# Performance work log

Measured on AMD Instinct MI355X. Metric: run time of the kernel, lower is better.

The kernel has to match this reference:

```python
import jax, jax.numpy as jnp
import numpy as np
from jax import lax

B, CIN, HID, T, H, W = 4, 16, 16, 31, 128, 128


def setup_inputs() -> dict:
    key = jax.random.key(0)
    k1, k2 = jax.random.split(key)
    X = jax.random.normal(k1, (B, CIN, T, H, W), dtype=jnp.float32)
    # conv weight: Conv3d(in=16, out=4*hidden=64, k=3, pad=1), fan-in scaled
    fan_in = CIN * 27
    Wt = jax.random.normal(k2, (4 * HID, CIN, 3, 3, 3), dtype=jnp.float32) / np.sqrt(fan_in)
    b = jnp.zeros((4 * HID,), dtype=jnp.float32)
    return {"X": X, "W": Wt, "b": b}


def reference(X, W, b):
    # conv step: [B, 4*HID, T, H, W]
    gates = lax.conv_general_dilated(
        X, W, window_strides=(1, 1, 1), padding="SAME",
        dimension_numbers=("NCDHW", "OIDHW", "NCDHW"))
    gates = gates + b[None, :, None, None, None]
    Z, F, O, I = jnp.split(gates, 4, axis=1)
    Z = jnp.tanh(Z)
    F = jax.nn.sigmoid(F)
    O = jax.nn.sigmoid(O)
    I = jax.nn.sigmoid(I)

    # linear recurrence over time (axis=2), forward direction:
    # c_t = f_t * c_{t-1} + i_t * z_t  (c_{-1} = 0), h_t = o_t * c_t
    Zt = jnp.moveaxis(Z, 2, 0)  # [T, B, HID, H, W]
    Ft = jnp.moveaxis(F, 2, 0)
    Ot = jnp.moveaxis(O, 2, 0)
    It = jnp.moveaxis(I, 2, 0)

    def step(c, zfio):
        z, f, o, i = zfio
        c_ = f * c + i * z
        return c_, o * c_

    c0 = jnp.zeros_like(Zt[0])
    _, hs = lax.scan(step, c0, (Zt, Ft, Ot, It))
    return jnp.moveaxis(hs, 0, 2)  # [B, HID, T, H, W]
```

## Files before the change

kernel.cpp:

```cpp
#include <hip/hip_runtime.h>
#include <math.h>

#define Bn   4
#define CINn 16
#define HIDn 16
#define Tn   31
#define Hn   128
#define Wn   128

#define NS   14

typedef _Float16 half8 __attribute__((ext_vector_type(8)));
typedef float    f32x4 __attribute__((ext_vector_type(4)));

constexpr int KDt[28] = {0,0,0,0,0,0,0,0,0, 1,1,1,1,1,1,1,1,1, 2,2,2,2,2,2,2,2,2, 2};
constexpr int KHt[28] = {0,0,0,1,1,1,2,2,2, 0,0,0,1,1,1,2,2,2, 0,0,0,1,1,1,2,2,2, 2};
constexpr int KWt[28] = {0,1,2,0,1,2,0,1,2, 0,1,2,0,1,2,0,1,2, 0,1,2,0,1,2,0,1,2, 2};

__device__ __forceinline__ float sigmoidf_(float x) { return 1.f / (1.f + __expf(-x)); }
__device__ __forceinline__ float tanhf_(float x)    { return 2.f / (1.f + __expf(-2.f * x)) - 1.f; }

__global__ void repack_wa_kernel(const float* __restrict__ W, _Float16* __restrict__ WA) {
    int idx = blockIdx.x * blockDim.x + threadIdx.x;
    if (idx >= NS * 4 * 64 * 8) return;
    int j    = idx & 7;
    int lane = (idx >> 3) & 63;
    int m    = (idx >> 9) & 3;
    int s    = idx >> 11;
    int g    = lane >> 4;
    int tap  = 2 * s + (g >> 1);
    int cin  = (g & 1) * 8 + j;
    int oc   = m * 16 + (lane & 15);
    float v  = (tap < 27) ? W[(size_t)(oc * CINn + cin) * 27 + tap] : 0.f;
    WA[idx] = (_Float16)v;
}

#define POSB    48
#define NWPOS   66
#define ROWF    (NWPOS*POSB)
#define SLOTF   (3*ROWF)
#define LDSF    (4*SLOTF)
#define NPOS    (3*NWPOS)
#define XH_OFF  65536
#define SLICE_B (Hn*Wn*CINn*2)
#define WS_NEED ((size_t)XH_OFF + (size_t)Bn*Tn*SLICE_B)

__global__ __launch_bounds__(256)
void transpose_x_kernel(const float* __restrict__ X, _Float16* __restrict__ Xh) {
    int i   = blockIdx.x * 256 + threadIdx.x;
    int pos = i & 16383;
    int bu  = i >> 14;
    int b   = bu / 31;
    int u   = bu - b * 31;
    const float* src = X + ((size_t)(b * CINn) * Tn + u) * 16384 + pos;
    half8 h0, h1;
    #pragma unroll
    for (int c = 0; c < 8; c++) h0[c] = (_Float16)src[(size_t)c * (Tn * 16384)];
    #pragma unroll
    for (int c = 0; c < 8; c++) h1[c] = (_Float16)src[(size_t)(c + 8) * (Tn * 16384)];
    half8* dst = (half8*)(Xh + (size_t)i * 16);
    dst[0] = h0; dst[1] = h1;
}

__global__ __launch_bounds__(256, 2)
void qrnn_xh_kernel(const _Float16* __restrict__ Xh, const _Float16* __restrict__ WA,
                    const float* __restrict__ bias, float* __restrict__ out) {
    __shared__ __align__(16) char smem[LDSF];

    const int tid  = threadIdx.x;
    const int lane = tid & 63;
    const int wv   = tid >> 6;

    const int swz = (blockIdx.x & 7) * 128 + (blockIdx.x >> 3);
    const int b    = swz >> 8;
    const int h    = (swz >> 1) & 127;
    const int wh   = swz & 1;
    const int woff = wh * 64;

    const size_t strideT = (size_t)Hn * Wn;
    const size_t strideC = (size_t)Tn * strideT;

    const int lane15 = lane & 15;
    const int g      = lane >> 4;
    const int ghi    = g >> 1;
    const int e      = g & 1;
    const int wloc   = wv * 16 + lane15;
    const int pbase  = wloc * POSB + e * 16;

    float bz[4], bfv[4], bov[4], biv[4];
    #pragma unroll
    for (int r = 0; r < 4; r++) {
        int hid = g * 4 + r;
        bz[r]  = bias[hid];
        bfv[r] = bias[HIDn + hid];
        bov[r] = bias[2 * HIDn + hid];
        biv[r] = bias[3 * HIDn + hid];
    }

    const char* XhB = (const char*)Xh + (size_t)b * Tn * SLICE_B;
    const bool own  = (tid < NPOS);
    const int  srow = tid / NWPOS;
    const int  swp  = tid - srow * NWPOS;
    const int  hr   = h - 1 + srow;
    const int  wa   = woff - 1 + swp;
    const bool inb  = own && (hr >= 0) && (hr < Hn) && (wa >= 0) && (wa < Wn);
    const int  soff = (hr * Wn + wa) * 32;
    const int  loff = srow * ROWF + swp * POSB;

    half8 pfA, pfB;

    auto issue = [&](int u) {
        half8 a = {}, c = {};
        if (inb && u >= 0 && u < Tn) {
            const char* s = XhB + (size_t)u * SLICE_B + soff;
            a = *reinterpret_cast<const half8*>(s);
            c = *reinterpret_cast<const half8*>(s + 16);
        }
        pfA = a; pfB = c;
    };
    auto commit = [&](int u) {
        if (own) {
            char* dst = smem + (u & 3) * SLOTF + loff;
            *reinterpret_cast<half8*>(dst)      = pfA;
            *reinterpret_cast<half8*>(dst + 16) = pfB;
        }
    };

    if (own) {
        half8 z = {};
        char* dst = smem + 3 * SLOTF + loff;
        *reinterpret_cast<half8*>(dst)      = z;
        *reinterpret_cast<half8*>(dst + 16) = z;
    }
    issue(0);
    commit(0);
    issue(1);

    float cst[4] = {0.f, 0.f, 0.f, 0.f};
    float* outb = out + (size_t)b * HIDn * strideC + (size_t)h * Wn + woff + wloc;

    for (int t = 0; t < Tn; t++) {
        commit(t + 1);
        __syncthreads();
        issue(t + 2);

        const int sb[3] = { ((t + 3) & 3) * SLOTF, (t & 3) * SLOTF, ((t + 1) & 3) * SLOTF };

        f32x4 acc[4];
        #pragma unroll
        for (int m = 0; m < 4; m++) acc[m] = (f32x4)(0.f);

        #pragma unroll
        for (int s = 0; s < NS; s++) {
            const half8 a0 = *reinterpret_cast<const half8*>(WA + ((size_t)(s * 4 + 0) * 64 + lane) * 8);
            const half8 a1 = *reinterpret_cast<const half8*>(WA + ((size_t)(s * 4 + 1) * 64 + lane) * 8);
            const half8 a2 = *reinterpret_cast<const half8*>(WA + ((size_t)(s * 4 + 2) * 64 + lane) * 8);
            const half8 a3 = *reinterpret_cast<const half8*>(WA + ((size_t)(s * 4 + 3) * 64 + lane) * 8);

            const int tA = 2 * s, tB = 2 * s + 1;
            const int offA = sb[KDt[tA]] + KHt[tA] * ROWF + KWt[tA] * POSB;
            const int offB = sb[KDt[tB]] + KHt[tB] * ROWF + KWt[tB] * POSB;
            const int off  = (ghi ? offB : offA) + pbase;

            const half8 bf = *reinterpret_cast<const half8*>(smem + off);
            acc[0] = __builtin_amdgcn_mfma_f32_16x16x32_f16(a0, bf, acc[0], 0, 0, 0);
            acc[1] = __builtin_amdgcn_mfma_f32_16x16x32_f16(a1, bf, acc[1], 0, 0, 0);
            acc[2] = __builtin_amdgcn_mfma_f32_16x16x32_f16(a2, bf, acc[2], 0, 0, 0);
            acc[3] = __builtin_amdgcn_mfma_f32_16x16x32_f16(a3, bf, acc[3], 0, 0, 0);
        }

        #pragma unroll
        for (int r = 0; r < 4; r++) {
            float z = tanhf_   (acc[0][r] + bz[r]);
            float f = sigmoidf_(acc[1][r] + bfv[r]);
            float o = sigmoidf_(acc[2][r] + bov[r]);
            float i = sigmoidf_(acc[3][r] + biv[r]);
            float c = f * cst[r] + i * z;
            cst[r] = c;
            outb[(size_t)(g * 4 + r) * strideC + (size_t)t * strideT] = o * c;
        }
    }
}

#define WSTR  48
#define ROWB  (130*WSTR)
#define SLOT3 (3*ROWB)
#define LDS3  (3*SLOT3)

__global__ __launch_bounds__(256, 2)
void qrnn_fb_kernel(const float* __restrict__ X, const _Float16* __restrict__ WA,
                    const float* __restrict__ bias, float* __restrict__ out) {
    __shared__ __align__(16) char smem[LDS3];
    const int tid  = threadIdx.x;
    const int lane = tid & 63;
    const int wv   = tid >> 6;
    const int swz = (blockIdx.x & 7) * 64 + (blockIdx.x >> 3);
    const int b = swz >> 7;
    const int h = swz & 127;
    const size_t strideT = (size_t)Hn * Wn;
    const size_t strideC = (size_t)Tn * strideT;
    const float* Xb = X + (size_t)b * CINn * strideC;
    const int lane15  = lane & 15;
    const int g       = lane >> 4;
    const int ghi     = g >> 1;
    const int laneoff = lane15 * WSTR + (g & 1) * 16;
    const int wbase   = wv * 32;
    float bz[4], bfv[4], bov[4], biv[4];
    #pragma unroll
    for (int r = 0; r < 4; r++) {
        int hid = g * 4 + r;
        bz[r] = bias[hid]; bfv[r] = bias[HIDn + hid];
        bov[r] = bias[2 * HIDn + hid]; biv[r] = bias[3 * HIDn + hid];
    }
    auto stage = [&](int u, int s) {
        const bool uok = (u >= 0) && (u < Tn);
        for (int p = tid; p < 3 * 130; p += 256) {
            int row  = (p >= 260) ? 2 : (p >= 130) ? 1 : 0;
            int wpos = p - row * 130;
            int hr = h - 1 + row;
            int wa = wpos - 1;
            bool valid = uok && (hr >= 0) && (hr < Hn) && (wa >= 0) && (wa < Wn);
            const float* src = Xb + (ptrdiff_t)u * (ptrdiff_t)strideT + (ptrdiff_t)hr * Wn + wa;
            half8 h0, h1;
            #pragma unroll
            for (int c8 = 0; c8 < 8; c8++) h0[c8] = valid ? (_Float16)src[(size_t)c8 * strideC] : (_Float16)0.f;
            #pragma unroll
            for (int c8 = 0; c8 < 8; c8++) h1[c8] = valid ? (_Float16)src[(size_t)(8 + c8) * strideC] : (_Float16)0.f;
            char* dst = smem + s * SLOT3 + row * ROWB + wpos * WSTR;
            *reinterpret_cast<half8*>(dst)      = h0;
            *reinterpret_cast<half8*>(dst + 16) = h1;
        }
    };
    float cst[2][4];
    #pragma unroll
    for (int n = 0; n < 2; n++)
        #pragma unroll
        for (int r = 0; r < 4; r++) cst[n][r] = 0.f;
    stage(-1, 2);
    stage(0, 0);
    float* outb = out + (size_t)b * HIDn * strideC + (size_t)h * Wn + wbase + lane15;
    for (int t = 0; t < Tn; t++) {
        stage(t + 1, (t + 1) % 3);
        __syncthreads();
        const int sb[3] = { ((t + 2) % 3) * SLOT3, (t % 3) * SLOT3, ((t + 1) % 3) * SLOT3 };
        f32x4 acc[2][4];
        #pragma unroll
        for (int n = 0; n < 2; n++)
            #pragma unroll
            for (int m = 0; m < 4; m++) acc[n][m] = (f32x4)(0.f);
        #pragma unroll
        for (int s = 0; s < NS; s++) {
            const half8 a0 = *reinterpret_cast<const half8*>(WA + ((size_t)(s * 4 + 0) * 64 + lane) * 8);
            const half8 a1 = *reinterpret_cast<const half8*>(WA + ((size_t)(s * 4 + 1) * 64 + lane) * 8);
            const half8 a2 = *reinterpret_cast<const half8*>(WA + ((size_t)(s * 4 + 2) * 64 + lane) * 8);
            const half8 a3 = *reinterpret_cast<const half8*>(WA + ((size_t)(s * 4 + 3) * 64 + lane) * 8);
            const int tA = 2 * s, tB = 2 * s + 1;
            const int offA = sb[KDt[tA]] + KHt[tA] * ROWB + KWt[tA] * WSTR;
            const int offB = sb[KDt[tB]] + KHt[tB] * ROWB + KWt[tB] * WSTR;
            const int off  = (ghi ? offB : offA) + laneoff;
            #pragma unroll
            for (int n = 0; n < 2; n++) {
                const half8 bf = *reinterpret_cast<const half8*>(smem + off + (wbase + n * 16) * WSTR);
                acc[n][0] = __builtin_amdgcn_mfma_f32_16x16x32_f16(a0, bf, acc[n][0], 0, 0, 0);
                acc[n][1] = __builtin_amdgcn_mfma_f32_16x16x32_f16(a1, bf, acc[n][1], 0, 0, 0);
                acc[n][2] = __builtin_amdgcn_mfma_f32_16x16x32_f16(a2, bf, acc[n][2], 0, 0, 0);
                acc[n][3] = __builtin_amdgcn_mfma_f32_16x16x32_f16(a3, bf, acc[n][3], 0, 0, 0);
            }
        }
        #pragma unroll
        for (int n = 0; n < 2; n++) {
            #pragma unroll
            for (int r = 0; r < 4; r++) {
                float z = tanhf_   (acc[n][0][r] + bz[r]);
                float f = sigmoidf_(acc[n][1][r] + bfv[r]);
                float o = sigmoidf_(acc[n][2][r] + bov[r]);
                float i = sigmoidf_(acc[n][3][r] + biv[r]);
                float c = f * cst[n][r] + i * z;
                cst[n][r] = c;
                outb[(size_t)(g * 4 + r) * strideC + (size_t)t * strideT + n * 16] = o * c;
            }
        }
        __syncthreads();
    }
}

extern "C" void kernel_launch(void* const* d_in, const int* in_sizes, int n_in,
                              void* d_out, int out_size, void* d_ws, size_t ws_size,
                              hipStream_t stream) {
    const float* X    = (const float*)d_in[0];
    const float* W    = (const float*)d_in[1];
    const float* bias = (const float*)d_in[2];
    float* out = (float*)d_out;

    _Float16* WA = (_Float16*)d_ws;
    repack_wa_kernel<<<(NS * 4 * 64 * 8 + 255) / 256, 256, 0, stream>>>(W, WA);

    if (ws_size >= WS_NEED) {
        _Float16* Xh = (_Float16*)((char*)d_ws + XH_OFF);
        transpose_x_kernel<<<(Bn * Tn * Hn * Wn) / 256, 256, 0, stream>>>(X, Xh);
        qrnn_xh_kernel<<<Bn * Hn * 2, 256, 0, stream>>>(Xh, WA, bias, out);
    } else {
        qrnn_fb_kernel<<<Bn * Hn, 256, 0, stream>>>(X, WA, bias, out);
    }
}
```

Baseline: 486.2 us.

## Halve the QRNN block width and fold the bias into an extra MFMA step

The main kernel now uses 128-thread blocks that each cover 32 output columns instead of 64, launching four blocks per row with a new swizzle and a narrower LDS halo tile. The goal is more resident blocks per CU and cheaper per-step barriers. The bias is written into the repacked weights as a 15th K-step, multiplied by a constant one-hot vector held in LDS, so the per-gate bias registers and adds disappear. In exchange each time step issues four extra MFMAs, and the halo overhead relative to useful columns rises.

```diff
diff --git a/kernel.cpp b/kernel.cpp
--- a/kernel.cpp
+++ b/kernel.cpp
@@ -8,7 +8,7 @@
 #define Hn   128
 #define Wn   128
 
-#define NS   14
+#define NS15 15
 
 typedef _Float16 half8 __attribute__((ext_vector_type(8)));
 typedef float    f32x4 __attribute__((ext_vector_type(4)));
@@ -20,9 +20,10 @@
 __device__ __forceinline__ float sigmoidf_(float x) { return 1.f / (1.f + __expf(-x)); }
 __device__ __forceinline__ float tanhf_(float x)    { return 2.f / (1.f + __expf(-2.f * x)) - 1.f; }
 
-__global__ void repack_wa_kernel(const float* __restrict__ W, _Float16* __restrict__ WA) {
+__global__ void repack_wa_kernel(const float* __restrict__ W, const float* __restrict__ bias,
+                                 _Float16* __restrict__ WA) {
     int idx = blockIdx.x * blockDim.x + threadIdx.x;
-    if (idx >= NS * 4 * 64 * 8) return;
+    if (idx >= NS15 * 4 * 64 * 8) return;
     int j    = idx & 7;
     int lane = (idx >> 3) & 63;
     int m    = (idx >> 9) & 3;
@@ -31,15 +32,18 @@
     int tap  = 2 * s + (g >> 1);
     int cin  = (g & 1) * 8 + j;
     int oc   = m * 16 + (lane & 15);
-    float v  = (tap < 27) ? W[(size_t)(oc * CINn + cin) * 27 + tap] : 0.f;
+    float v  = 0.f;
+    if (tap < 27)                    v = W[(size_t)(oc * CINn + cin) * 27 + tap];
+    else if (tap == 28 && cin == 0)  v = bias[oc];
     WA[idx] = (_Float16)v;
 }
 
 #define POSB    48
-#define NWPOS   66
+#define NWPOS   34
 #define ROWF    (NWPOS*POSB)
 #define SLOTF   (3*ROWF)
-#define LDSF    (4*SLOTF)
+#define CONSTO  (4*SLOTF)
+#define LDSF    (CONSTO + 64)
 #define NPOS    (3*NWPOS)
 #define XH_OFF  65536
 #define SLICE_B (Hn*Wn*CINn*2)
@@ -62,20 +66,20 @@
     dst[0] = h0; dst[1] = h1;
 }
 
-__global__ __launch_bounds__(256, 2)
-void qrnn_xh_kernel(const _Float16* __restrict__ Xh, const _Float16* __restrict__ WA,
-                    const float* __restrict__ bias, float* __restrict__ out) {
+__global__ __launch_bounds__(128, 4)
+void qrnn_q_kernel(const _Float16* __restrict__ Xh, const _Float16* __restrict__ WA,
+                   float* __restrict__ out) {
     __shared__ __align__(16) char smem[LDSF];
 
     const int tid  = threadIdx.x;
     const int lane = tid & 63;
     const int wv   = tid >> 6;
 
-    const int swz = (blockIdx.x & 7) * 128 + (blockIdx.x >> 3);
-    const int b    = swz >> 8;
-    const int h    = (swz >> 1) & 127;
-    const int wh   = swz & 1;
-    const int woff = wh * 64;
+    const int swz = (blockIdx.x & 7) * 256 + (blockIdx.x >> 3);
+    const int b    = swz >> 9;
+    const int h    = (swz >> 2) & 127;
+    const int wq   = swz & 3;
+    const int woff = wq * 32;
 
     const size_t strideT = (size_t)Hn * Wn;
     const size_t strideC = (size_t)Tn * strideT;
@@ -87,15 +91,7 @@
     const int wloc   = wv * 16 + lane15;
     const int pbase  = wloc * POSB + e * 16;
 
-    float bz[4], bfv[4], bov[4], biv[4];
-    #pragma unroll
-    for (int r = 0; r < 4; r++) {
-        int hid = g * 4 + r;
-        bz[r]  = bias[hid];
-        bfv[r] = bias[HIDn + hid];
-        bov[r] = bias[2 * HIDn + hid];
-        biv[r] = bias[3 * HIDn + hid];
-    }
+    if (tid < 32) ((unsigned short*)(smem + CONSTO))[tid] = (tid == 0) ? 0x3C00 : 0;
 
     const char* XhB = (const char*)Xh + (size_t)b * Tn * SLICE_B;
     const bool own  = (tid < NPOS);
@@ -151,7 +147,7 @@
         for (int m = 0; m < 4; m++) acc[m] = (f32x4)(0.f);
 
         #pragma unroll
-        for (int s = 0; s < NS; s++) {
+        for (int s = 0; s < 14; s++) {
             const half8 a0 = *reinterpret_cast<const half8*>(WA + ((size_t)(s * 4 + 0) * 64 + lane) * 8);
             const half8 a1 = *reinterpret_cast<const half8*>(WA + ((size_t)(s * 4 + 1) * 64 + lane) * 8);
             const half8 a2 = *reinterpret_cast<const half8*>(WA + ((size_t)(s * 4 + 2) * 64 + lane) * 8);
@@ -168,13 +164,24 @@
             acc[2] = __builtin_amdgcn_mfma_f32_16x16x32_f16(a2, bf, acc[2], 0, 0, 0);
             acc[3] = __builtin_amdgcn_mfma_f32_16x16x32_f16(a3, bf, acc[3], 0, 0, 0);
         }
+        {
+            const half8 a0 = *reinterpret_cast<const half8*>(WA + ((size_t)(14 * 4 + 0) * 64 + lane) * 8);
+            const half8 a1 = *reinterpret_cast<const half8*>(WA + ((size_t)(14 * 4 + 1) * 64 + lane) * 8);
+            const half8 a2 = *reinterpret_cast<const half8*>(WA + ((size_t)(14 * 4 + 2) * 64 + lane) * 8);
+            const half8 a3 = *reinterpret_cast<const half8*>(WA + ((size_t)(14 * 4 + 3) * 64 + lane) * 8);
+            const half8 bf = *reinterpret_cast<const half8*>(smem + CONSTO + (ghi * 2 + e) * 16);
+            acc[0] = __builtin_amdgcn_mfma_f32_16x16x32_f16(a0, bf, acc[0], 0, 0, 0);
+            acc[1] = __builtin_amdgcn_mfma_f32_16x16x32_f16(a1, bf, acc[1], 0, 0, 0);
+            acc[2] = __builtin_amdgcn_mfma_f32_16x16x32_f16(a2, bf, acc[2], 0, 0, 0);
+            acc[3] = __builtin_amdgcn_mfma_f32_16x16x32_f16(a3, bf, acc[3], 0, 0, 0);
+        }
 
         #pragma unroll
         for (int r = 0; r < 4; r++) {
-            float z = tanhf_   (acc[0][r] + bz[r]);
-            float f = sigmoidf_(acc[1][r] + bfv[r]);
-            float o = sigmoidf_(acc[2][r] + bov[r]);
-            float i = sigmoidf_(acc[3][r] + biv[r]);
+            float z = tanhf_   (acc[0][r]);
+            float f = sigmoidf_(acc[1][r]);
+            float o = sigmoidf_(acc[2][r]);
+            float i = sigmoidf_(acc[3][r]);
             float c = f * cst[r] + i * z;
             cst[r] = c;
             outb[(size_t)(g * 4 + r) * strideC + (size_t)t * strideT] = o * c;
@@ -249,7 +256,7 @@
             #pragma unroll
             for (int m = 0; m < 4; m++) acc[n][m] = (f32x4)(0.f);
         #pragma unroll
-        for (int s = 0; s < NS; s++) {
+        for (int s = 0; s < 14; s++) {
             const half8 a0 = *reinterpret_cast<const half8*>(WA + ((size_t)(s * 4 + 0) * 64 + lane) * 8);
             const half8 a1 = *reinterpret_cast<const half8*>(WA + ((size_t)(s * 4 + 1) * 64 + lane) * 8);
             const half8 a2 = *reinterpret_cast<const half8*>(WA + ((size_t)(s * 4 + 2) * 64 + lane) * 8);
@@ -293,12 +300,12 @@
     float* out = (float*)d_out;
 
     _Float16* WA = (_Float16*)d_ws;
-    repack_wa_kernel<<<(NS * 4 * 64 * 8 + 255) / 256, 256, 0, stream>>>(W, WA);
+    repack_wa_kernel<<<(NS15 * 4 * 64 * 8 + 255) / 256, 256, 0, stream>>>(W, bias, WA);
 
     if (ws_size >= WS_NEED) {
         _Float16* Xh = (_Float16*)((char*)d_ws + XH_OFF);
         transpose_x_kernel<<<(Bn * Tn * Hn * Wn) / 256, 256, 0, stream>>>(X, Xh);
-        qrnn_xh_kernel<<<Bn * Hn * 2, 256, 0, stream>>>(Xh, WA, bias, out);
+        qrnn_q_kernel<<<Bn * Hn * 4, 128, 0, stream>>>(Xh, WA, out);
     } else {
         qrnn_fb_kernel<<<Bn * Hn, 256, 0, stream>>>(X, WA, bias, out);
     }
```

Result: slower. 1.002 ms (+106.1%).
